# Kernel optimization log

Measured on AMD Instinct MI355X. Metric: run time of the kernel, lower is better.

Reference implementation:

```python
import jax, jax.numpy as jnp
import numpy as np

N_NODES = 50000
N_EDGES = 600000
N_GRAPHS = 1000
IN_DIM = 16
HID = 128
DESC = 17
NUM_LAYERS = 3
BN_EPS = 1e-5


def setup_inputs() -> dict:
    key = jax.random.key(0)
    ks = jax.random.split(key, 16)
    x = jax.random.normal(ks[0], (N_NODES, IN_DIM), dtype=jnp.float32)
    edge_index = jax.random.randint(ks[1], (2, N_EDGES), 0, N_NODES, dtype=jnp.int32)
    edge_attr = jax.random.normal(ks[2], (N_EDGES, HID), dtype=jnp.float32)
    batch = jnp.sort(jax.random.randint(ks[3], (N_NODES,), 0, N_GRAPHS, dtype=jnp.int32))
    mol_desc = jax.random.normal(ks[4], (N_GRAPHS, DESC), dtype=jnp.float32)
    s = 1.0 / np.sqrt(HID)
    Wp = jax.random.normal(ks[5], (IN_DIM, HID), dtype=jnp.float32) / np.sqrt(IN_DIM)
    bp = jnp.zeros((HID,), jnp.float32)
    W1 = jax.random.normal(ks[6], (NUM_LAYERS, HID, HID), dtype=jnp.float32) * s
    b1 = jnp.zeros((NUM_LAYERS, HID), jnp.float32)
    W2 = jax.random.normal(ks[7], (NUM_LAYERS, HID, HID), dtype=jnp.float32) * s
    b2 = jnp.zeros((NUM_LAYERS, HID), jnp.float32)
    gamma = jnp.ones((NUM_LAYERS, HID), jnp.float32)
    beta = jnp.zeros((NUM_LAYERS, HID), jnp.float32)
    Wf = jax.random.normal(ks[8], (HID + DESC, 1), dtype=jnp.float32) / np.sqrt(HID + DESC)
    bf = jnp.zeros((1,), jnp.float32)
    return dict(x=x, edge_index=edge_index, edge_attr=edge_attr, batch=batch,
                mol_desc=mol_desc, Wp=Wp, bp=bp, W1=W1, b1=b1, W2=W2, b2=b2,
                gamma=gamma, beta=beta, Wf=Wf, bf=bf)


def reference(x, edge_index, edge_attr, batch, mol_desc,
              Wp, bp, W1, b1, W2, b2, gamma, beta, Wf, bf):
    src, dst = edge_index[0], edge_index[1]
    h = x @ Wp + bp  # [N, HID]
    for l in range(NUM_LAYERS):
        # GINEConv: aggr_i = sum_j relu(h_j + e_ij); out = MLP((1+eps)*h + aggr), eps=0
        msg = jax.nn.relu(h[src] + edge_attr)                       # [E, HID] gather
        aggr = jax.ops.segment_sum(msg, dst, num_segments=N_NODES)  # scatter-add
        z = h + aggr
        z = jax.nn.relu(z @ W1[l] + b1[l]) @ W2[l] + b2[l]
        # BatchNorm1d (training-mode batch statistics)
        mean = jnp.mean(z, axis=0)
        var = jnp.var(z, axis=0)
        z = (z - mean) * jax.lax.rsqrt(var + BN_EPS) * gamma[l] + beta[l]
        h = jax.nn.relu(z)  # dropout = identity (eval)
    # global mean pool per graph
    sums = jax.ops.segment_sum(h, batch, num_segments=N_GRAPHS)
    counts = jax.ops.segment_sum(jnp.ones((N_NODES,), h.dtype), batch, num_segments=N_GRAPHS)
    pooled = sums / jnp.maximum(counts, 1.0)[:, None]
    feats = jnp.concatenate([pooled, mol_desc], axis=1)  # [G, HID+DESC]
    return (feats @ Wf + bf).squeeze(-1)  # [G]
```

## Files before the change

kernel.cpp:

```cpp
#include <hip/hip_runtime.h>
#include <hip/hip_bf16.h>

#define NN 50000
#define NE 600000
#define NG 1000
#define IND 16
#define HID 128
#define DESCD 17
#define NL 3
#define BN_EPS 1e-5f
#define NB_SCAN 196

typedef short s16x8 __attribute__((ext_vector_type(8)));
typedef float f32x4 __attribute__((ext_vector_type(4)));
typedef float f32x2 __attribute__((ext_vector_type(2)));
typedef __hip_bfloat16 bfp16;
typedef __hip_bfloat162 bfp162;

__global__ __launch_bounds__(256) void k_hist(const int* __restrict__ dst,
                                              int* __restrict__ deg) {
    int e = blockIdx.x * blockDim.x + threadIdx.x;
    if (e >= NE) return;
    atomicAdd(&deg[dst[e]], 1);
}

__global__ __launch_bounds__(256) void k_part(const int* __restrict__ deg,
                                              int* __restrict__ partials) {
    __shared__ int sh[256];
    int i = blockIdx.x * 256 + threadIdx.x;
    sh[threadIdx.x] = (i < NN) ? deg[i] : 0;
    __syncthreads();
    for (int o = 128; o > 0; o >>= 1) {
        if (threadIdx.x < o) sh[threadIdx.x] += sh[threadIdx.x + o];
        __syncthreads();
    }
    if (threadIdx.x == 0) partials[blockIdx.x] = sh[0];
}

__global__ __launch_bounds__(256) void k_scanpart(const int* __restrict__ partials,
                                                  int* __restrict__ poffs) {
    __shared__ int sh[256];
    int t = threadIdx.x;
    int v = (t < NB_SCAN) ? partials[t] : 0;
    sh[t] = v;
    __syncthreads();
    for (int o = 1; o < 256; o <<= 1) {
        int tmp = (t >= o) ? sh[t - o] : 0;
        __syncthreads();
        sh[t] += tmp;
        __syncthreads();
    }
    if (t < NB_SCAN) poffs[t] = sh[t] - v;
}

__global__ __launch_bounds__(256) void k_scatter(const int* __restrict__ deg,
                                                 const int* __restrict__ poffs,
                                                 int* __restrict__ rowptr,
                                                 int* __restrict__ cursor) {
    __shared__ int sh[256];
    int b = blockIdx.x, t = threadIdx.x;
    int i = b * 256 + t;
    int v = (i < NN) ? deg[i] : 0;
    sh[t] = v;
    __syncthreads();
    for (int o = 1; o < 256; o <<= 1) {
        int tmp = (t >= o) ? sh[t - o] : 0;
        __syncthreads();
        sh[t] += tmp;
        __syncthreads();
    }
    int excl = sh[t] - v + poffs[b];
    if (i < NN) {
        rowptr[i] = excl;
        cursor[i] = excl;
        if (i == NN - 1) rowptr[NN] = excl + v;
    }
}

__global__ __launch_bounds__(256) void k_fill(const int* __restrict__ src,
                                              const int* __restrict__ dst,
                                              int* __restrict__ cursor,
                                              int2* __restrict__ perm) {
    int e = blockIdx.x * blockDim.x + threadIdx.x;
    if (e >= NE) return;
    int pos = atomicAdd(&cursor[dst[e]], 1);
    perm[pos] = make_int2(e, src[e]);
}

__global__ __launch_bounds__(256) void k_wprep(const float* __restrict__ W1,
                                               const float* __restrict__ W2,
                                               bfp16* __restrict__ Wt) {
    int id = blockIdx.x * blockDim.x + threadIdx.x;
    if (id >= 6 * HID * HID) return;
    int m = id >> 14;
    int rem = id & 16383;
    int n = rem >> 7, k = rem & 127;
    const float* Wsrc = (m < 3) ? (W1 + (size_t)m * HID * HID)
                                : (W2 + (size_t)(m - 3) * HID * HID);
    Wt[id] = __float2bfloat16(Wsrc[k * HID + n]);
}

__global__ __launch_bounds__(256) void k_proj(const float* __restrict__ x,
                                              const float* __restrict__ Wp,
                                              const float* __restrict__ bp,
                                              bfp16* __restrict__ h) {
    int idx = blockIdx.x * blockDim.x + threadIdx.x;
    if (idx >= NN * HID) return;
    int row = idx >> 7, col = idx & 127;
    const float* xr = x + (size_t)row * IND;
    float acc = bp[col];
#pragma unroll
    for (int k = 0; k < IND; k++) acc += xr[k] * Wp[k * HID + col];
    h[idx] = __float2bfloat16(acc);
}

template <int MODE, bool BN>
__global__ __launch_bounds__(256) void k_aggr(const bfp16* __restrict__ hz,
                                              const float* __restrict__ ea,
                                              bfp162* __restrict__ eab2,
                                              const int2* __restrict__ perm,
                                              const int* __restrict__ rowptr,
                                              const float* __restrict__ stats,
                                              const float* __restrict__ gamma,
                                              const float* __restrict__ beta,
                                              bfp16* __restrict__ z) {
    int nid = (blockIdx.x * blockDim.x + threadIdx.x) >> 6;
    int lane = threadIdx.x & 63;
    if (nid >= NN) return;
    const int f = lane * 2;

    float sc0 = 0.f, sf0 = 0.f, sc1 = 0.f, sf1 = 0.f;
    if (BN) {
        const float invn = 1.f / NN;
        float m0 = stats[f] * invn;
        float v0 = stats[128 + f] * invn - m0 * m0;
        sc0 = rsqrtf(v0 + BN_EPS) * gamma[f];
        sf0 = beta[f] - m0 * sc0;
        float m1 = stats[f + 1] * invn;
        float v1 = stats[128 + f + 1] * invn - m1 * m1;
        sc1 = rsqrtf(v1 + BN_EPS) * gamma[f + 1];
        sf1 = beta[f + 1] - m1 * sc1;
    }

    int beg = rowptr[nid], end = rowptr[nid + 1];
    float ax = 0.f, ay = 0.f;
    int i = beg;
    for (; i + 3 < end; i += 4) {
#pragma unroll
        for (int u = 0; u < 4; u++) {
            int2 pr = perm[i + u];
            float2 a;
            if (MODE == 2) {
                a = __bfloat1622float2(eab2[(size_t)(i + u) * 64 + lane]);
            } else {
                f32x2 av = __builtin_nontemporal_load(
                        (const f32x2*)&ea[(size_t)pr.x * HID + f]);
                a = make_float2(av.x, av.y);
                eab2[(size_t)(i + u) * 64 + lane] = __float22bfloat162_rn(a);
            }
            float2 hv = __bfloat1622float2(*(const bfp162*)&hz[(size_t)pr.y * HID + f]);
            if (BN) {
                hv.x = fmaxf(hv.x * sc0 + sf0, 0.f);
                hv.y = fmaxf(hv.y * sc1 + sf1, 0.f);
            }
            ax += fmaxf(a.x + hv.x, 0.f);
            ay += fmaxf(a.y + hv.y, 0.f);
        }
    }
    for (; i < end; i++) {
        int2 pr = perm[i];
        float2 a;
        if (MODE == 2) {
            a = __bfloat1622float2(eab2[(size_t)i * 64 + lane]);
        } else {
            f32x2 av = __builtin_nontemporal_load(
                    (const f32x2*)&ea[(size_t)pr.x * HID + f]);
            a = make_float2(av.x, av.y);
            eab2[(size_t)i * 64 + lane] = __float22bfloat162_rn(a);
        }
        float2 hv = __bfloat1622float2(*(const bfp162*)&hz[(size_t)pr.y * HID + f]);
        if (BN) {
            hv.x = fmaxf(hv.x * sc0 + sf0, 0.f);
            hv.y = fmaxf(hv.y * sc1 + sf1, 0.f);
        }
        ax += fmaxf(a.x + hv.x, 0.f);
        ay += fmaxf(a.y + hv.y, 0.f);
    }
    float2 hn = __bfloat1622float2(*(const bfp162*)&hz[(size_t)nid * HID + f]);
    if (BN) {
        hn.x = fmaxf(hn.x * sc0 + sf0, 0.f);
        hn.y = fmaxf(hn.y * sc1 + sf1, 0.f);
    }
    *(bfp162*)&z[(size_t)nid * HID + f] =
        __float22bfloat162_rn(make_float2(ax + hn.x, ay + hn.y));
}

__global__ __launch_bounds__(256) void k_mlp(const bfp16* __restrict__ A,
                                             const bfp16* __restrict__ Wt1,
                                             const bfp16* __restrict__ Wt2,
                                             const float* __restrict__ b1,
                                             const float* __restrict__ b2,
                                             bfp16* __restrict__ z2,
                                             float* __restrict__ stats,
                                             int N) {
    __shared__ __align__(16) short sW1[128 * 128];
    __shared__ __align__(16) short sW2[128 * 128];
    __shared__ __align__(16) short sA[64 * 128];
    const int t = threadIdx.x;
    const int rowBase = blockIdx.x * 64;

    const short* W1g = (const short*)Wt1;
    const short* W2g = (const short*)Wt2;
    for (int g = t; g < 2048; g += 256) {
        int nrow = g >> 4, s = g & 15;
        int sw = nrow * 128 + ((s ^ (nrow & 7)) << 3);
        *(float4*)&sW1[sw] = *(const float4*)&W1g[g * 8];
        *(float4*)&sW2[sw] = *(const float4*)&W2g[g * 8];
    }
    const short* Ag = (const short*)A;
    for (int g = t; g < 1024; g += 256) {
        int r = g >> 4, s = g & 15;
        float4 v = make_float4(0.f, 0.f, 0.f, 0.f);
        if (rowBase + r < N) v = *(const float4*)&Ag[(size_t)(rowBase + r) * 128 + s * 8];
        *(float4*)&sA[r * 128 + ((s ^ (r & 7)) << 3)] = v;
    }
    __syncthreads();

    const int w = t >> 6, lane = t & 63;
    const int l15 = lane & 15, lhi = lane >> 4;
    const int arow = (w << 4) + l15;
    const int abase = arow * 128, asw = arow & 7;
    const int bsw = l15 & 7;

    f32x4 acc[8];
#pragma unroll
    for (int c = 0; c < 8; c++) acc[c] = (f32x4){0.f, 0.f, 0.f, 0.f};
#pragma unroll
    for (int kk = 0; kk < 4; kk++) {
        int kslot = kk * 4 + lhi;
        s16x8 af = *(const s16x8*)&sA[abase + ((kslot ^ asw) << 3)];
#pragma unroll
        for (int c = 0; c < 8; c++) {
            s16x8 bfr = *(const s16x8*)&sW1[(c * 16 + l15) * 128 + ((kslot ^ bsw) << 3)];
            acc[c] = __builtin_amdgcn_mfma_f32_16x16x32_bf16(af, bfr, acc[c], 0, 0, 0);
        }
    }
    __syncthreads();

    {
        const int rowb = (w << 4);
#pragma unroll
        for (int c = 0; c < 8; c++) {
            float bb = b1[c * 16 + l15];
            int col = c * 16 + l15;
#pragma unroll
            for (int r = 0; r < 4; r++) {
                int row = rowb + lhi * 4 + r;
                float v = fmaxf(acc[c][r] + bb, 0.f);
                bfp16 bv = __float2bfloat16(v);
                sA[row * 128 + ((((col >> 3)) ^ (row & 7)) << 3) + (col & 7)] =
                    *reinterpret_cast<short*>(&bv);
            }
        }
    }
    __syncthreads();

    f32x4 acc2[8];
#pragma unroll
    for (int c = 0; c < 8; c++) acc2[c] = (f32x4){0.f, 0.f, 0.f, 0.f};
#pragma unroll
    for (int kk = 0; kk < 4; kk++) {
        int kslot = kk * 4 + lhi;
        s16x8 af = *(const s16x8*)&sA[abase + ((kslot ^ asw) << 3)];
#pragma unroll
        for (int c = 0; c < 8; c++) {
            s16x8 bfr = *(const s16x8*)&sW2[(c * 16 + l15) * 128 + ((kslot ^ bsw) << 3)];
            acc2[c] = __builtin_amdgcn_mfma_f32_16x16x32_bf16(af, bfr, acc2[c], 0, 0, 0);
        }
    }

    const int rb = rowBase + (w << 4) + lhi * 4;
    float scol[8], qcol[8];
#pragma unroll
    for (int c = 0; c < 8; c++) {
        float bb = b2[c * 16 + l15];
        float s = 0.f, q = 0.f;
#pragma unroll
        for (int r = 0; r < 4; r++) {
            int row = rb + r;
            float v = acc2[c][r] + bb;
            if (row < N) {
                z2[(size_t)row * 128 + c * 16 + l15] = __float2bfloat16(v);
                s += v;
                q += v * v;
            }
        }
        scol[c] = s;
        qcol[c] = q;
    }
#pragma unroll
    for (int c = 0; c < 8; c++) {
        scol[c] += __shfl_xor(scol[c], 16);
        scol[c] += __shfl_xor(scol[c], 32);
        qcol[c] += __shfl_xor(qcol[c], 16);
        qcol[c] += __shfl_xor(qcol[c], 32);
    }
    __syncthreads();
    float* sStat = (float*)sA;
    if (lane < 16) {
#pragma unroll
        for (int c = 0; c < 8; c++) {
            sStat[w * 256 + c * 16 + lane] = scol[c];
            sStat[w * 256 + 128 + c * 16 + lane] = qcol[c];
        }
    }
    __syncthreads();
    if (t < 128) {
        float ss = sStat[t] + sStat[256 + t] + sStat[512 + t] + sStat[768 + t];
        float qq = sStat[128 + t] + sStat[384 + t] + sStat[640 + t] + sStat[896 + t];
        atomicAdd(&stats[t], ss);
        atomicAdd(&stats[128 + t], qq);
    }
}

__global__ __launch_bounds__(256) void k_finalpool(const bfp16* __restrict__ z2,
                                                   const float* __restrict__ stats,
                                                   const float* __restrict__ gamma,
                                                   const float* __restrict__ beta,
                                                   const int* __restrict__ batch,
                                                   const float* __restrict__ mol,
                                                   const float* __restrict__ Wf,
                                                   const float* __restrict__ bfp,
                                                   float* __restrict__ out) {
    int gid = (blockIdx.x * blockDim.x + threadIdx.x) >> 6;
    int lane = threadIdx.x & 63;
    if (gid >= NG) return;
    const int f = lane * 2;

    const float invn = 1.f / NN;
    float m0 = stats[f] * invn;
    float v0 = stats[128 + f] * invn - m0 * m0;
    float sc0 = rsqrtf(v0 + BN_EPS) * gamma[f];
    float sf0 = beta[f] - m0 * sc0;
    float m1 = stats[f + 1] * invn;
    float v1 = stats[128 + f + 1] * invn - m1 * m1;
    float sc1 = rsqrtf(v1 + BN_EPS) * gamma[f + 1];
    float sf1 = beta[f + 1] - m1 * sc1;

    int lo = 0, hi = NN;
    while (lo < hi) { int m = (lo + hi) >> 1; if (batch[m] < gid) lo = m + 1; else hi = m; }
    int lb = lo;
    hi = NN;
    while (lo < hi) { int m = (lo + hi) >> 1; if (batch[m] <= gid) lo = m + 1; else hi = m; }
    int cnt = lo - lb;

    float sx = 0.f, sy = 0.f;
    for (int n = lb; n < lo; n++) {
        float2 v = __bfloat1622float2(*(const bfp162*)&z2[(size_t)n * HID + f]);
        sx += fmaxf(v.x * sc0 + sf0, 0.f);
        sy += fmaxf(v.y * sc1 + sf1, 0.f);
    }
    float inv = 1.f / fmaxf((float)cnt, 1.f);
    float acc = sx * inv * Wf[f] + sy * inv * Wf[f + 1];
    if (lane < DESCD) acc += mol[(size_t)gid * DESCD + lane] * Wf[HID + lane];
#pragma unroll
    for (int o = 32; o > 0; o >>= 1) acc += __shfl_down(acc, o);
    if (lane == 0) out[gid] = acc + bfp[0];
}

extern "C" void kernel_launch(void* const* d_in, const int* in_sizes, int n_in,
                              void* d_out, int out_size, void* d_ws, size_t ws_size,
                              hipStream_t stream) {
    const float* x     = (const float*)d_in[0];
    const int*   ei    = (const int*)d_in[1];
    const float* ea    = (const float*)d_in[2];
    const int*   batch = (const int*)d_in[3];
    const float* mol   = (const float*)d_in[4];
    const float* Wp    = (const float*)d_in[5];
    const float* bp    = (const float*)d_in[6];
    const float* W1    = (const float*)d_in[7];
    const float* b1    = (const float*)d_in[8];
    const float* W2    = (const float*)d_in[9];
    const float* b2    = (const float*)d_in[10];
    const float* gamma = (const float*)d_in[11];
    const float* beta  = (const float*)d_in[12];
    const float* Wf    = (const float*)d_in[13];
    const float* bf_   = (const float*)d_in[14];
    float* out = (float*)d_out;

    char* p = (char*)d_ws;
    size_t off = 0;
    auto alloc = [&](size_t bytes) {
        char* q = p + off;
        off = (off + bytes + 255) & ~(size_t)255;
        return q;
    };
    bfp16* h      = (bfp16*)alloc((size_t)NN * HID * 2);
    bfp16* z      = (bfp16*)alloc((size_t)NN * HID * 2);
    bfp16* z2     = (bfp16*)alloc((size_t)NN * HID * 2);
    bfp16* Wt     = (bfp16*)alloc((size_t)6 * HID * HID * 2);
    int2*  perm   = (int2*)alloc((size_t)NE * 8);
    int*   rowptr = (int*)alloc((NN + 16) * 4);
    int*   cursor = (int*)alloc(NN * 4);
    int*   partials = (int*)alloc(NB_SCAN * 4);
    int*   poffs    = (int*)alloc(NB_SCAN * 4);
    size_t zoff = off;
    int*   deg    = (int*)alloc(NN * 4);
    float* stats3 = (float*)alloc(3 * 256 * 4);
    size_t zlen = off - zoff;
    bfp162* eab2 = (bfp162*)alloc((size_t)NE * HID * 2);

    const int* src = ei;
    const int* dst = ei + NE;

    (void)hipMemsetAsync(p + zoff, 0, zlen, stream);
    k_hist<<<(NE + 255) / 256, 256, 0, stream>>>(dst, deg);
    k_part<<<NB_SCAN, 256, 0, stream>>>(deg, partials);
    k_scanpart<<<1, 256, 0, stream>>>(partials, poffs);
    k_scatter<<<NB_SCAN, 256, 0, stream>>>(deg, poffs, rowptr, cursor);
    k_fill<<<(NE + 255) / 256, 256, 0, stream>>>(src, dst, cursor, perm);
    k_wprep<<<(6 * HID * HID + 255) / 256, 256, 0, stream>>>(W1, W2, Wt);
    k_proj<<<(NN * HID) / 256, 256, 0, stream>>>(x, Wp, bp, h);

    const int aggrGrid = (NN * 64) / 256;
    const int mlpGrid = (NN + 63) / 64;
    for (int l = 0; l < NL; l++) {
        if (l == 0)
            k_aggr<1, false><<<aggrGrid, 256, 0, stream>>>(
                h, ea, eab2, perm, rowptr, nullptr, nullptr, nullptr, z);
        else
            k_aggr<2, true><<<aggrGrid, 256, 0, stream>>>(
                z2, nullptr, eab2, perm, rowptr, stats3 + (l - 1) * 256,
                gamma + (l - 1) * HID, beta + (l - 1) * HID, z);
        k_mlp<<<mlpGrid, 256, 0, stream>>>(
            z, Wt + (size_t)l * HID * HID, Wt + (size_t)(3 + l) * HID * HID,
            b1 + l * HID, b2 + l * HID, z2, stats3 + l * 256, NN);
    }

    k_finalpool<<<(NG * 64) / 256, 256, 0, stream>>>(
        z2, stats3 + 2 * 256, gamma + 2 * HID, beta + 2 * HID,
        batch, mol, Wf, bf_, out);
}
```

Before: 431.8 us.

## Convert edge features to bf16 in CSR order with a streaming kernel, merge prep kernels

Edge attributes were previously gathered randomly in fp32 inside the first aggregation layer and written out as bf16. A new kernel now reads them sequentially with wide nontemporal loads and scatters bf16 rows into CSR order, using a per-edge position array. All three aggregation layers then read contiguous bf16 edge data, and the perm array shrinks to source indices only. The projection and weight-prep kernels are merged into one launch to save launch overhead. The cost is an extra kernel pass with scattered 256-byte writes.

```diff
diff --git a/kernel.cpp b/kernel.cpp
--- a/kernel.cpp
+++ b/kernel.cpp
@@ -13,7 +13,6 @@
 
 typedef short s16x8 __attribute__((ext_vector_type(8)));
 typedef float f32x4 __attribute__((ext_vector_type(4)));
-typedef float f32x2 __attribute__((ext_vector_type(2)));
 typedef __hip_bfloat16 bfp16;
 typedef __hip_bfloat162 bfp162;
 
@@ -80,45 +79,67 @@
 __global__ __launch_bounds__(256) void k_fill(const int* __restrict__ src,
                                               const int* __restrict__ dst,
                                               int* __restrict__ cursor,
-                                              int2* __restrict__ perm) {
+                                              int* __restrict__ epos,
+                                              int* __restrict__ sperm) {
     int e = blockIdx.x * blockDim.x + threadIdx.x;
     if (e >= NE) return;
     int pos = atomicAdd(&cursor[dst[e]], 1);
-    perm[pos] = make_int2(e, src[e]);
-}
-
-__global__ __launch_bounds__(256) void k_wprep(const float* __restrict__ W1,
-                                               const float* __restrict__ W2,
-                                               bfp16* __restrict__ Wt) {
-    int id = blockIdx.x * blockDim.x + threadIdx.x;
-    if (id >= 6 * HID * HID) return;
-    int m = id >> 14;
-    int rem = id & 16383;
-    int n = rem >> 7, k = rem & 127;
-    const float* Wsrc = (m < 3) ? (W1 + (size_t)m * HID * HID)
-                                : (W2 + (size_t)(m - 3) * HID * HID);
-    Wt[id] = __float2bfloat16(Wsrc[k * HID + n]);
-}
-
-__global__ __launch_bounds__(256) void k_proj(const float* __restrict__ x,
-                                              const float* __restrict__ Wp,
-                                              const float* __restrict__ bp,
-                                              bfp16* __restrict__ h) {
-    int idx = blockIdx.x * blockDim.x + threadIdx.x;
-    if (idx >= NN * HID) return;
-    int row = idx >> 7, col = idx & 127;
-    const float* xr = x + (size_t)row * IND;
-    float acc = bp[col];
-#pragma unroll
-    for (int k = 0; k < IND; k++) acc += xr[k] * Wp[k * HID + col];
-    h[idx] = __float2bfloat16(acc);
-}
-
-template <int MODE, bool BN>
+    epos[e] = pos;
+    sperm[pos] = src[e];
+}
+
+__global__ __launch_bounds__(256) void k_conv(const float* __restrict__ ea,
+                                              const int* __restrict__ epos,
+                                              bfp16* __restrict__ eab) {
+    int t = blockIdx.x * 256 + threadIdx.x;
+    int e = t >> 4;
+    if (e >= NE) return;
+    int f = (t & 15) << 3;
+    const f32x4* src = (const f32x4*)&ea[(size_t)e * HID + f];
+    f32x4 a = __builtin_nontemporal_load(src);
+    f32x4 b = __builtin_nontemporal_load(src + 1);
+    bfp162 p0 = __float22bfloat162_rn(make_float2(a.x, a.y));
+    bfp162 p1 = __float22bfloat162_rn(make_float2(a.z, a.w));
+    bfp162 p2 = __float22bfloat162_rn(make_float2(b.x, b.y));
+    bfp162 p3 = __float22bfloat162_rn(make_float2(b.z, b.w));
+    int pos = epos[e];
+    bfp162* dstp = (bfp162*)&eab[(size_t)pos * HID + f];
+    dstp[0] = p0; dstp[1] = p1; dstp[2] = p2; dstp[3] = p3;
+}
+
+__global__ __launch_bounds__(256) void k_projwprep(const float* __restrict__ x,
+                                                   const float* __restrict__ Wp,
+                                                   const float* __restrict__ bp,
+                                                   bfp16* __restrict__ h,
+                                                   const float* __restrict__ W1,
+                                                   const float* __restrict__ W2,
+                                                   bfp16* __restrict__ Wt,
+                                                   int projBlocks) {
+    if (blockIdx.x < (unsigned)projBlocks) {
+        int idx = blockIdx.x * blockDim.x + threadIdx.x;
+        if (idx >= NN * HID) return;
+        int row = idx >> 7, col = idx & 127;
+        const float* xr = x + (size_t)row * IND;
+        float acc = bp[col];
+#pragma unroll
+        for (int k = 0; k < IND; k++) acc += xr[k] * Wp[k * HID + col];
+        h[idx] = __float2bfloat16(acc);
+    } else {
+        int id = (blockIdx.x - projBlocks) * blockDim.x + threadIdx.x;
+        if (id >= 6 * HID * HID) return;
+        int m = id >> 14;
+        int rem = id & 16383;
+        int n = rem >> 7, k = rem & 127;
+        const float* Wsrc = (m < 3) ? (W1 + (size_t)m * HID * HID)
+                                    : (W2 + (size_t)(m - 3) * HID * HID);
+        Wt[id] = __float2bfloat16(Wsrc[k * HID + n]);
+    }
+}
+
+template <bool BN>
 __global__ __launch_bounds__(256) void k_aggr(const bfp16* __restrict__ hz,
-                                              const float* __restrict__ ea,
-                                              bfp162* __restrict__ eab2,
-                                              const int2* __restrict__ perm,
+                                              const bfp16* __restrict__ eab,
+                                              const int* __restrict__ sperm,
                                               const int* __restrict__ rowptr,
                                               const float* __restrict__ stats,
                                               const float* __restrict__ gamma,
@@ -148,17 +169,9 @@
     for (; i + 3 < end; i += 4) {
 #pragma unroll
         for (int u = 0; u < 4; u++) {
-            int2 pr = perm[i + u];
-            float2 a;
-            if (MODE == 2) {
-                a = __bfloat1622float2(eab2[(size_t)(i + u) * 64 + lane]);
-            } else {
-                f32x2 av = __builtin_nontemporal_load(
-                        (const f32x2*)&ea[(size_t)pr.x * HID + f]);
-                a = make_float2(av.x, av.y);
-                eab2[(size_t)(i + u) * 64 + lane] = __float22bfloat162_rn(a);
-            }
-            float2 hv = __bfloat1622float2(*(const bfp162*)&hz[(size_t)pr.y * HID + f]);
+            float2 a = __bfloat1622float2(*(const bfp162*)&eab[(size_t)(i + u) * HID + f]);
+            int s = sperm[i + u];
+            float2 hv = __bfloat1622float2(*(const bfp162*)&hz[(size_t)s * HID + f]);
             if (BN) {
                 hv.x = fmaxf(hv.x * sc0 + sf0, 0.f);
                 hv.y = fmaxf(hv.y * sc1 + sf1, 0.f);
@@ -168,17 +181,9 @@
         }
     }
     for (; i < end; i++) {
-        int2 pr = perm[i];
-        float2 a;
-        if (MODE == 2) {
-            a = __bfloat1622float2(eab2[(size_t)i * 64 + lane]);
-        } else {
-            f32x2 av = __builtin_nontemporal_load(
-                    (const f32x2*)&ea[(size_t)pr.x * HID + f]);
-            a = make_float2(av.x, av.y);
-            eab2[(size_t)i * 64 + lane] = __float22bfloat162_rn(a);
-        }
-        float2 hv = __bfloat1622float2(*(const bfp162*)&hz[(size_t)pr.y * HID + f]);
+        float2 a = __bfloat1622float2(*(const bfp162*)&eab[(size_t)i * HID + f]);
+        int s = sperm[i];
+        float2 hv = __bfloat1622float2(*(const bfp162*)&hz[(size_t)s * HID + f]);
         if (BN) {
             hv.x = fmaxf(hv.x * sc0 + sf0, 0.f);
             hv.y = fmaxf(hv.y * sc1 + sf1, 0.f);
@@ -399,7 +404,8 @@
     bfp16* z      = (bfp16*)alloc((size_t)NN * HID * 2);
     bfp16* z2     = (bfp16*)alloc((size_t)NN * HID * 2);
     bfp16* Wt     = (bfp16*)alloc((size_t)6 * HID * HID * 2);
-    int2*  perm   = (int2*)alloc((size_t)NE * 8);
+    int*   epos   = (int*)alloc((size_t)NE * 4);
+    int*   sperm  = (int*)alloc((size_t)NE * 4);
     int*   rowptr = (int*)alloc((NN + 16) * 4);
     int*   cursor = (int*)alloc(NN * 4);
     int*   partials = (int*)alloc(NB_SCAN * 4);
@@ -408,7 +414,7 @@
     int*   deg    = (int*)alloc(NN * 4);
     float* stats3 = (float*)alloc(3 * 256 * 4);
     size_t zlen = off - zoff;
-    bfp162* eab2 = (bfp162*)alloc((size_t)NE * HID * 2);
+    bfp16* eab = (bfp16*)alloc((size_t)NE * HID * 2);
 
     const int* src = ei;
     const int* dst = ei + NE;
@@ -418,19 +424,24 @@
     k_part<<<NB_SCAN, 256, 0, stream>>>(deg, partials);
     k_scanpart<<<1, 256, 0, stream>>>(partials, poffs);
     k_scatter<<<NB_SCAN, 256, 0, stream>>>(deg, poffs, rowptr, cursor);
-    k_fill<<<(NE + 255) / 256, 256, 0, stream>>>(src, dst, cursor, perm);
-    k_wprep<<<(6 * HID * HID + 255) / 256, 256, 0, stream>>>(W1, W2, Wt);
-    k_proj<<<(NN * HID) / 256, 256, 0, stream>>>(x, Wp, bp, h);
+    k_fill<<<(NE + 255) / 256, 256, 0, stream>>>(src, dst, cursor, epos, sperm);
+    k_conv<<<(NE * 16) / 256, 256, 0, stream>>>(ea, epos, eab);
+    {
+        const int projBlocks = (NN * HID) / 256;
+        const int wprepBlocks = (6 * HID * HID + 255) / 256;
+        k_projwprep<<<projBlocks + wprepBlocks, 256, 0, stream>>>(
+            x, Wp, bp, h, W1, W2, Wt, projBlocks);
+    }
 
     const int aggrGrid = (NN * 64) / 256;
     const int mlpGrid = (NN + 63) / 64;
     for (int l = 0; l < NL; l++) {
         if (l == 0)
-            k_aggr<1, false><<<aggrGrid, 256, 0, stream>>>(
-                h, ea, eab2, perm, rowptr, nullptr, nullptr, nullptr, z);
+            k_aggr<false><<<aggrGrid, 256, 0, stream>>>(
+                h, eab, sperm, rowptr, nullptr, nullptr, nullptr, z);
         else
-            k_aggr<2, true><<<aggrGrid, 256, 0, stream>>>(
-                z2, nullptr, eab2, perm, rowptr, stats3 + (l - 1) * 256,
+            k_aggr<true><<<aggrGrid, 256, 0, stream>>>(
+                z2, eab, sperm, rowptr, stats3 + (l - 1) * 256,
                 gamma + (l - 1) * HID, beta + (l - 1) * HID, z);
         k_mlp<<<mlpGrid, 256, 0, stream>>>(
             z, Wt + (size_t)l * HID * HID, Wt + (size_t)(3 + l) * HID * HID,
```

Measured after the change: 460.3 us. +6.6%, slower.

## Merge CSR build into cooperative kernel and pre-convert edge attrs to bf16

Applied to the files above, without the earlier changes.

Folds the memset, histogram, scans and fill passes into one cooperative kernel that uses grid-wide syncs, cutting several launches. Edge attributes are converted to bf16 in original edge order by a streaming prep kernel that also does projection and weight transposition. Aggregation then gathers bf16 edge attributes by edge id in every layer instead of reading them sequentially in CSR order from a permuted copy. This removes the fp32 gather in layer 0, but layers 1-2 now do random 256-byte gathers where they previously did sequential reads.

```diff
diff --git a/kernel.cpp b/kernel.cpp
--- a/kernel.cpp
+++ b/kernel.cpp
@@ -1,5 +1,8 @@
 #include <hip/hip_runtime.h>
+#include <hip/hip_cooperative_groups.h>
 #include <hip/hip_bf16.h>
+
+namespace cg = cooperative_groups;
 
 #define NN 50000
 #define NE 600000
@@ -9,115 +12,125 @@
 #define DESCD 17
 #define NL 3
 #define BN_EPS 1e-5f
-#define NB_SCAN 196
+#define NCH 196
 
 typedef short s16x8 __attribute__((ext_vector_type(8)));
 typedef float f32x4 __attribute__((ext_vector_type(4)));
 typedef float f32x2 __attribute__((ext_vector_type(2)));
+typedef int   i32x4 __attribute__((ext_vector_type(4)));
 typedef __hip_bfloat16 bfp16;
 typedef __hip_bfloat162 bfp162;
 
-__global__ __launch_bounds__(256) void k_hist(const int* __restrict__ dst,
-                                              int* __restrict__ deg) {
-    int e = blockIdx.x * blockDim.x + threadIdx.x;
-    if (e >= NE) return;
-    atomicAdd(&deg[dst[e]], 1);
-}
-
-__global__ __launch_bounds__(256) void k_part(const int* __restrict__ deg,
-                                              int* __restrict__ partials) {
+struct CsrPrm {
+    const int* src; const int* dst;
+    int2* perm; int* rowptr; int* cursor; int* partials; int* poffs; int* deg;
+    float* stats3;
+};
+
+__global__ void __launch_bounds__(256) k_csr(CsrPrm p) {
     __shared__ int sh[256];
-    int i = blockIdx.x * 256 + threadIdx.x;
-    sh[threadIdx.x] = (i < NN) ? deg[i] : 0;
-    __syncthreads();
-    for (int o = 128; o > 0; o >>= 1) {
-        if (threadIdx.x < o) sh[threadIdx.x] += sh[threadIdx.x + o];
+    cg::grid_group gg = cg::this_grid();
+    const int t = threadIdx.x;
+    const int bid = blockIdx.x;
+    const int nthr = gridDim.x * 256;
+    const int gtid = bid * 256 + t;
+
+    for (int i = gtid; i < NN; i += nthr) p.deg[i] = 0;
+    for (int i = gtid; i < 3 * 256; i += nthr) p.stats3[i] = 0.f;
+    gg.sync();
+    for (int e = gtid; e < NE; e += nthr) atomicAdd(&p.deg[p.dst[e]], 1);
+    gg.sync();
+    if (bid < NCH) {
+        int i = bid * 256 + t;
+        int v = (i < NN) ? p.deg[i] : 0;
+        sh[t] = v;
         __syncthreads();
-    }
-    if (threadIdx.x == 0) partials[blockIdx.x] = sh[0];
-}
-
-__global__ __launch_bounds__(256) void k_scanpart(const int* __restrict__ partials,
-                                                  int* __restrict__ poffs) {
-    __shared__ int sh[256];
-    int t = threadIdx.x;
-    int v = (t < NB_SCAN) ? partials[t] : 0;
-    sh[t] = v;
-    __syncthreads();
-    for (int o = 1; o < 256; o <<= 1) {
-        int tmp = (t >= o) ? sh[t - o] : 0;
+        for (int o = 1; o < 256; o <<= 1) {
+            int tmp = (t >= o) ? sh[t - o] : 0;
+            __syncthreads();
+            sh[t] += tmp;
+            __syncthreads();
+        }
+        if (i < NN) p.rowptr[i] = sh[t] - v;
+        if (t == 255) p.partials[bid] = sh[255];
+    }
+    gg.sync();
+    if (bid == 0) {
+        int v = (t < NCH) ? p.partials[t] : 0;
+        sh[t] = v;
         __syncthreads();
-        sh[t] += tmp;
-        __syncthreads();
-    }
-    if (t < NB_SCAN) poffs[t] = sh[t] - v;
-}
-
-__global__ __launch_bounds__(256) void k_scatter(const int* __restrict__ deg,
-                                                 const int* __restrict__ poffs,
-                                                 int* __restrict__ rowptr,
-                                                 int* __restrict__ cursor) {
-    __shared__ int sh[256];
-    int b = blockIdx.x, t = threadIdx.x;
-    int i = b * 256 + t;
-    int v = (i < NN) ? deg[i] : 0;
-    sh[t] = v;
-    __syncthreads();
-    for (int o = 1; o < 256; o <<= 1) {
-        int tmp = (t >= o) ? sh[t - o] : 0;
-        __syncthreads();
-        sh[t] += tmp;
-        __syncthreads();
-    }
-    int excl = sh[t] - v + poffs[b];
-    if (i < NN) {
-        rowptr[i] = excl;
-        cursor[i] = excl;
-        if (i == NN - 1) rowptr[NN] = excl + v;
-    }
-}
-
-__global__ __launch_bounds__(256) void k_fill(const int* __restrict__ src,
-                                              const int* __restrict__ dst,
-                                              int* __restrict__ cursor,
-                                              int2* __restrict__ perm) {
-    int e = blockIdx.x * blockDim.x + threadIdx.x;
-    if (e >= NE) return;
-    int pos = atomicAdd(&cursor[dst[e]], 1);
-    perm[pos] = make_int2(e, src[e]);
-}
-
-__global__ __launch_bounds__(256) void k_wprep(const float* __restrict__ W1,
-                                               const float* __restrict__ W2,
-                                               bfp16* __restrict__ Wt) {
-    int id = blockIdx.x * blockDim.x + threadIdx.x;
-    if (id >= 6 * HID * HID) return;
-    int m = id >> 14;
-    int rem = id & 16383;
-    int n = rem >> 7, k = rem & 127;
-    const float* Wsrc = (m < 3) ? (W1 + (size_t)m * HID * HID)
-                                : (W2 + (size_t)(m - 3) * HID * HID);
-    Wt[id] = __float2bfloat16(Wsrc[k * HID + n]);
-}
-
-__global__ __launch_bounds__(256) void k_proj(const float* __restrict__ x,
+        for (int o = 1; o < 256; o <<= 1) {
+            int tmp = (t >= o) ? sh[t - o] : 0;
+            __syncthreads();
+            sh[t] += tmp;
+            __syncthreads();
+        }
+        if (t < NCH) p.poffs[t] = sh[t] - v;
+    }
+    gg.sync();
+    if (bid < NCH) {
+        int i = bid * 256 + t;
+        if (i < NN) {
+            int r = p.rowptr[i] + p.poffs[bid];
+            p.rowptr[i] = r;
+            p.cursor[i] = r;
+            if (i == NN - 1) p.rowptr[NN] = r + p.deg[i];
+        }
+    }
+    gg.sync();
+    for (int e = gtid; e < NE; e += nthr) {
+        int pos = atomicAdd(&p.cursor[p.dst[e]], 1);
+        p.perm[pos] = make_int2(e, p.src[e]);
+    }
+}
+
+__global__ __launch_bounds__(256) void k_prep(const float* __restrict__ ea,
+                                              bfp16* __restrict__ eab,
+                                              const float* __restrict__ x,
                                               const float* __restrict__ Wp,
                                               const float* __restrict__ bp,
-                                              bfp16* __restrict__ h) {
-    int idx = blockIdx.x * blockDim.x + threadIdx.x;
-    if (idx >= NN * HID) return;
-    int row = idx >> 7, col = idx & 127;
-    const float* xr = x + (size_t)row * IND;
-    float acc = bp[col];
-#pragma unroll
-    for (int k = 0; k < IND; k++) acc += xr[k] * Wp[k * HID + col];
-    h[idx] = __float2bfloat16(acc);
-}
-
-template <int MODE, bool BN>
+                                              bfp16* __restrict__ h,
+                                              const float* __restrict__ W1,
+                                              const float* __restrict__ W2,
+                                              bfp16* __restrict__ Wt) {
+    const size_t nthr = (size_t)gridDim.x * 256;
+    const size_t gt = (size_t)blockIdx.x * 256 + threadIdx.x;
+    const size_t nchunk = (size_t)NE * HID / 8;
+    for (size_t i = gt; i < nchunk; i += nthr) {
+        const f32x4* s = (const f32x4*)(ea + i * 8);
+        f32x4 a = __builtin_nontemporal_load(s);
+        f32x4 b = __builtin_nontemporal_load(s + 1);
+        bfp162 q0 = __float22bfloat162_rn(make_float2(a.x, a.y));
+        bfp162 q1 = __float22bfloat162_rn(make_float2(a.z, a.w));
+        bfp162 q2 = __float22bfloat162_rn(make_float2(b.x, b.y));
+        bfp162 q3 = __float22bfloat162_rn(make_float2(b.z, b.w));
+        i32x4 o;
+        o.x = *reinterpret_cast<int*>(&q0);
+        o.y = *reinterpret_cast<int*>(&q1);
+        o.z = *reinterpret_cast<int*>(&q2);
+        o.w = *reinterpret_cast<int*>(&q3);
+        __builtin_nontemporal_store(o, (i32x4*)(eab + i * 8));
+    }
+    for (size_t idx = gt; idx < (size_t)NN * HID; idx += nthr) {
+        int row = (int)(idx >> 7), col = (int)(idx & 127);
+        const float* xr = x + (size_t)row * IND;
+        float acc = bp[col];
+#pragma unroll
+        for (int k = 0; k < IND; k++) acc += xr[k] * Wp[k * HID + col];
+        h[idx] = __float2bfloat16(acc);
+    }
+    for (size_t id = gt; id < 6 * HID * HID; id += nthr) {
+        int m = (int)(id >> 14), rem = (int)(id & 16383);
+        int n = rem >> 7, k = rem & 127;
+        const float* Wsrc = (m < 3) ? (W1 + (size_t)m * HID * HID)
+                                    : (W2 + (size_t)(m - 3) * HID * HID);
+        Wt[id] = __float2bfloat16(Wsrc[k * HID + n]);
+    }
+}
+
+template <bool BN>
 __global__ __launch_bounds__(256) void k_aggr(const bfp16* __restrict__ hz,
-                                              const float* __restrict__ ea,
-                                              bfp162* __restrict__ eab2,
+                                              const bfp16* __restrict__ eab,
                                               const int2* __restrict__ perm,
                                               const int* __restrict__ rowptr,
                                               const float* __restrict__ stats,
@@ -149,15 +162,7 @@
 #pragma unroll
         for (int u = 0; u < 4; u++) {
             int2 pr = perm[i + u];
-            float2 a;
-            if (MODE == 2) {
-                a = __bfloat1622float2(eab2[(size_t)(i + u) * 64 + lane]);
-            } else {
-                f32x2 av = __builtin_nontemporal_load(
-                        (const f32x2*)&ea[(size_t)pr.x * HID + f]);
-                a = make_float2(av.x, av.y);
-                eab2[(size_t)(i + u) * 64 + lane] = __float22bfloat162_rn(a);
-            }
+            float2 a = __bfloat1622float2(*(const bfp162*)&eab[(size_t)pr.x * HID + f]);
             float2 hv = __bfloat1622float2(*(const bfp162*)&hz[(size_t)pr.y * HID + f]);
             if (BN) {
                 hv.x = fmaxf(hv.x * sc0 + sf0, 0.f);
@@ -169,15 +174,7 @@
     }
     for (; i < end; i++) {
         int2 pr = perm[i];
-        float2 a;
-        if (MODE == 2) {
-            a = __bfloat1622float2(eab2[(size_t)i * 64 + lane]);
-        } else {
-            f32x2 av = __builtin_nontemporal_load(
-                    (const f32x2*)&ea[(size_t)pr.x * HID + f]);
-            a = make_float2(av.x, av.y);
-            eab2[(size_t)i * 64 + lane] = __float22bfloat162_rn(a);
-        }
+        float2 a = __bfloat1622float2(*(const bfp162*)&eab[(size_t)pr.x * HID + f]);
         float2 hv = __bfloat1622float2(*(const bfp162*)&hz[(size_t)pr.y * HID + f]);
         if (BN) {
             hv.x = fmaxf(hv.x * sc0 + sf0, 0.f);
@@ -402,35 +399,40 @@
     int2*  perm   = (int2*)alloc((size_t)NE * 8);
     int*   rowptr = (int*)alloc((NN + 16) * 4);
     int*   cursor = (int*)alloc(NN * 4);
-    int*   partials = (int*)alloc(NB_SCAN * 4);
-    int*   poffs    = (int*)alloc(NB_SCAN * 4);
-    size_t zoff = off;
-    int*   deg    = (int*)alloc(NN * 4);
-    float* stats3 = (float*)alloc(3 * 256 * 4);
-    size_t zlen = off - zoff;
-    bfp162* eab2 = (bfp162*)alloc((size_t)NE * HID * 2);
-
-    const int* src = ei;
-    const int* dst = ei + NE;
-
-    (void)hipMemsetAsync(p + zoff, 0, zlen, stream);
-    k_hist<<<(NE + 255) / 256, 256, 0, stream>>>(dst, deg);
-    k_part<<<NB_SCAN, 256, 0, stream>>>(deg, partials);
-    k_scanpart<<<1, 256, 0, stream>>>(partials, poffs);
-    k_scatter<<<NB_SCAN, 256, 0, stream>>>(deg, poffs, rowptr, cursor);
-    k_fill<<<(NE + 255) / 256, 256, 0, stream>>>(src, dst, cursor, perm);
-    k_wprep<<<(6 * HID * HID + 255) / 256, 256, 0, stream>>>(W1, W2, Wt);
-    k_proj<<<(NN * HID) / 256, 256, 0, stream>>>(x, Wp, bp, h);
+    int*   partials = (int*)alloc(NCH * 4);
+    int*   poffs    = (int*)alloc(NCH * 4);
+    int*   deg      = (int*)alloc(NN * 4);
+    float* stats3   = (float*)alloc(3 * 256 * 4);
+    bfp16* eab      = (bfp16*)alloc((size_t)NE * HID * 2);
+
+    CsrPrm cp;
+    cp.src = ei; cp.dst = ei + NE;
+    cp.perm = perm; cp.rowptr = rowptr; cp.cursor = cursor;
+    cp.partials = partials; cp.poffs = poffs; cp.deg = deg; cp.stats3 = stats3;
+
+    int occ = 0;
+    if (hipOccupancyMaxActiveBlocksPerMultiprocessor(&occ, (const void*)k_csr, 256, 0)
+            != hipSuccess || occ <= 0)
+        occ = 4;
+    int csrGrid = occ * 256;
+    if (csrGrid > 784) csrGrid = 784;
+    if (csrGrid < NCH) csrGrid = NCH;
+
+    void* args[] = { &cp };
+    (void)hipLaunchCooperativeKernel((const void*)k_csr, dim3(csrGrid), dim3(256),
+                                     args, 0, stream);
+
+    k_prep<<<9600000 / 256, 256, 0, stream>>>(ea, eab, x, Wp, bp, h, W1, W2, Wt);
 
     const int aggrGrid = (NN * 64) / 256;
     const int mlpGrid = (NN + 63) / 64;
     for (int l = 0; l < NL; l++) {
         if (l == 0)
-            k_aggr<1, false><<<aggrGrid, 256, 0, stream>>>(
-                h, ea, eab2, perm, rowptr, nullptr, nullptr, nullptr, z);
+            k_aggr<false><<<aggrGrid, 256, 0, stream>>>(
+                h, eab, perm, rowptr, nullptr, nullptr, nullptr, z);
         else
-            k_aggr<2, true><<<aggrGrid, 256, 0, stream>>>(
-                z2, nullptr, eab2, perm, rowptr, stats3 + (l - 1) * 256,
+            k_aggr<true><<<aggrGrid, 256, 0, stream>>>(
+                z2, eab, perm, rowptr, stats3 + (l - 1) * 256,
                 gamma + (l - 1) * HID, beta + (l - 1) * HID, z);
         k_mlp<<<mlpGrid, 256, 0, stream>>>(
             z, Wt + (size_t)l * HID * HID, Wt + (size_t)(3 + l) * HID * HID,
```

Result: slower. 887.5 us (+105.5%).

## Pre-convert edge attributes to bf16 in a fused prep kernel

Applied to the files above, without the earlier changes.

Edge attributes are now converted from fp32 to bf16 in one streaming, fully coalesced pass inside a new k_prep kernel, which also does the input projection and the weight transpose. Previously the first aggregation layer gathered fp32 edge rows and wrote a bf16 copy in CSR order. All aggregation layers now read bf16 edge data gathered by the original edge id instead of sequentially in CSR order. This makes the first layer's gather cheaper and drops two launches, but gives up the contiguous streaming reads of edge data in layers two and three.

```diff
diff --git a/kernel.cpp b/kernel.cpp
--- a/kernel.cpp
+++ b/kernel.cpp
@@ -13,7 +13,7 @@
 
 typedef short s16x8 __attribute__((ext_vector_type(8)));
 typedef float f32x4 __attribute__((ext_vector_type(4)));
-typedef float f32x2 __attribute__((ext_vector_type(2)));
+typedef int   i32x4 __attribute__((ext_vector_type(4)));
 typedef __hip_bfloat16 bfp16;
 typedef __hip_bfloat162 bfp162;
 
@@ -87,37 +87,53 @@
     perm[pos] = make_int2(e, src[e]);
 }
 
-__global__ __launch_bounds__(256) void k_wprep(const float* __restrict__ W1,
-                                               const float* __restrict__ W2,
-                                               bfp16* __restrict__ Wt) {
-    int id = blockIdx.x * blockDim.x + threadIdx.x;
-    if (id >= 6 * HID * HID) return;
-    int m = id >> 14;
-    int rem = id & 16383;
-    int n = rem >> 7, k = rem & 127;
-    const float* Wsrc = (m < 3) ? (W1 + (size_t)m * HID * HID)
-                                : (W2 + (size_t)(m - 3) * HID * HID);
-    Wt[id] = __float2bfloat16(Wsrc[k * HID + n]);
-}
-
-__global__ __launch_bounds__(256) void k_proj(const float* __restrict__ x,
+__global__ __launch_bounds__(256) void k_prep(const float* __restrict__ ea,
+                                              bfp16* __restrict__ eab,
+                                              const float* __restrict__ x,
                                               const float* __restrict__ Wp,
                                               const float* __restrict__ bp,
-                                              bfp16* __restrict__ h) {
-    int idx = blockIdx.x * blockDim.x + threadIdx.x;
-    if (idx >= NN * HID) return;
-    int row = idx >> 7, col = idx & 127;
-    const float* xr = x + (size_t)row * IND;
-    float acc = bp[col];
-#pragma unroll
-    for (int k = 0; k < IND; k++) acc += xr[k] * Wp[k * HID + col];
-    h[idx] = __float2bfloat16(acc);
-}
-
-template <int MODE, bool BN>
+                                              bfp16* __restrict__ h,
+                                              const float* __restrict__ W1,
+                                              const float* __restrict__ W2,
+                                              bfp16* __restrict__ Wt) {
+    const size_t nthr = (size_t)gridDim.x * 256;
+    const size_t gt = (size_t)blockIdx.x * 256 + threadIdx.x;
+    const size_t nchunk = (size_t)NE * HID / 8;
+    for (size_t i = gt; i < nchunk; i += nthr) {
+        const f32x4* s = (const f32x4*)(ea + i * 8);
+        f32x4 a = __builtin_nontemporal_load(s);
+        f32x4 b = __builtin_nontemporal_load(s + 1);
+        bfp162 q0 = __float22bfloat162_rn(make_float2(a.x, a.y));
+        bfp162 q1 = __float22bfloat162_rn(make_float2(a.z, a.w));
+        bfp162 q2 = __float22bfloat162_rn(make_float2(b.x, b.y));
+        bfp162 q3 = __float22bfloat162_rn(make_float2(b.z, b.w));
+        i32x4 o;
+        o.x = *reinterpret_cast<int*>(&q0);
+        o.y = *reinterpret_cast<int*>(&q1);
+        o.z = *reinterpret_cast<int*>(&q2);
+        o.w = *reinterpret_cast<int*>(&q3);
+        __builtin_nontemporal_store(o, (i32x4*)(eab + i * 8));
+    }
+    for (size_t idx = gt; idx < (size_t)NN * HID; idx += nthr) {
+        int row = (int)(idx >> 7), col = (int)(idx & 127);
+        const float* xr = x + (size_t)row * IND;
+        float acc = bp[col];
+#pragma unroll
+        for (int k = 0; k < IND; k++) acc += xr[k] * Wp[k * HID + col];
+        h[idx] = __float2bfloat16(acc);
+    }
+    for (size_t id = gt; id < 6 * HID * HID; id += nthr) {
+        int m = (int)(id >> 14), rem = (int)(id & 16383);
+        int n = rem >> 7, k = rem & 127;
+        const float* Wsrc = (m < 3) ? (W1 + (size_t)m * HID * HID)
+                                    : (W2 + (size_t)(m - 3) * HID * HID);
+        Wt[id] = __float2bfloat16(Wsrc[k * HID + n]);
+    }
+}
+
+template <bool BN>
 __global__ __launch_bounds__(256) void k_aggr(const bfp16* __restrict__ hz,
-                                              const float* __restrict__ ea,
-                                              bfp162* __restrict__ eab2,
+                                              const bfp16* __restrict__ eab,
                                               const int2* __restrict__ perm,
                                               const int* __restrict__ rowptr,
                                               const float* __restrict__ stats,
@@ -149,15 +165,7 @@
 #pragma unroll
         for (int u = 0; u < 4; u++) {
             int2 pr = perm[i + u];
-            float2 a;
-            if (MODE == 2) {
-                a = __bfloat1622float2(eab2[(size_t)(i + u) * 64 + lane]);
-            } else {
-                f32x2 av = __builtin_nontemporal_load(
-                        (const f32x2*)&ea[(size_t)pr.x * HID + f]);
-                a = make_float2(av.x, av.y);
-                eab2[(size_t)(i + u) * 64 + lane] = __float22bfloat162_rn(a);
-            }
+            float2 a = __bfloat1622float2(*(const bfp162*)&eab[(size_t)pr.x * HID + f]);
             float2 hv = __bfloat1622float2(*(const bfp162*)&hz[(size_t)pr.y * HID + f]);
             if (BN) {
                 hv.x = fmaxf(hv.x * sc0 + sf0, 0.f);
@@ -169,15 +177,7 @@
     }
     for (; i < end; i++) {
         int2 pr = perm[i];
-        float2 a;
-        if (MODE == 2) {
-            a = __bfloat1622float2(eab2[(size_t)i * 64 + lane]);
-        } else {
-            f32x2 av = __builtin_nontemporal_load(
-                    (const f32x2*)&ea[(size_t)pr.x * HID + f]);
-            a = make_float2(av.x, av.y);
-            eab2[(size_t)i * 64 + lane] = __float22bfloat162_rn(a);
-        }
+        float2 a = __bfloat1622float2(*(const bfp162*)&eab[(size_t)pr.x * HID + f]);
         float2 hv = __bfloat1622float2(*(const bfp162*)&hz[(size_t)pr.y * HID + f]);
         if (BN) {
             hv.x = fmaxf(hv.x * sc0 + sf0, 0.f);
@@ -408,7 +408,7 @@
     int*   deg    = (int*)alloc(NN * 4);
     float* stats3 = (float*)alloc(3 * 256 * 4);
     size_t zlen = off - zoff;
-    bfp162* eab2 = (bfp162*)alloc((size_t)NE * HID * 2);
+    bfp16* eab    = (bfp16*)alloc((size_t)NE * HID * 2);
 
     const int* src = ei;
     const int* dst = ei + NE;
@@ -419,18 +419,17 @@
     k_scanpart<<<1, 256, 0, stream>>>(partials, poffs);
     k_scatter<<<NB_SCAN, 256, 0, stream>>>(deg, poffs, rowptr, cursor);
     k_fill<<<(NE + 255) / 256, 256, 0, stream>>>(src, dst, cursor, perm);
-    k_wprep<<<(6 * HID * HID + 255) / 256, 256, 0, stream>>>(W1, W2, Wt);
-    k_proj<<<(NN * HID) / 256, 256, 0, stream>>>(x, Wp, bp, h);
+    k_prep<<<9600000 / 256, 256, 0, stream>>>(ea, eab, x, Wp, bp, h, W1, W2, Wt);
 
     const int aggrGrid = (NN * 64) / 256;
     const int mlpGrid = (NN + 63) / 64;
     for (int l = 0; l < NL; l++) {
         if (l == 0)
-            k_aggr<1, false><<<aggrGrid, 256, 0, stream>>>(
-                h, ea, eab2, perm, rowptr, nullptr, nullptr, nullptr, z);
+            k_aggr<false><<<aggrGrid, 256, 0, stream>>>(
+                h, eab, perm, rowptr, nullptr, nullptr, nullptr, z);
         else
-            k_aggr<2, true><<<aggrGrid, 256, 0, stream>>>(
-                z2, nullptr, eab2, perm, rowptr, stats3 + (l - 1) * 256,
+            k_aggr<true><<<aggrGrid, 256, 0, stream>>>(
+                z2, eab, perm, rowptr, stats3 + (l - 1) * 256,
                 gamma + (l - 1) * HID, beta + (l - 1) * HID, z);
         k_mlp<<<mlpGrid, 256, 0, stream>>>(
             z, Wt + (size_t)l * HID * HID, Wt + (size_t)(3 + l) * HID * HID,
```

After: 457.7 us. 6.0% more time.
